# Optimization experiments

Hardware: AMD Instinct MI355X
Metric: run time of the kernel (lower is better)

Reference implementation:

```python
import jax, jax.numpy as jnp
import numpy as np

EMB_DIM = 128
MID = 192  # ceil(1.5 * emb_dim)
VOCAB = 3000
KCLS = 5
B = 16
S = 128
EPS = 1e-5


def _linear_init(k, fin, fout):
    k1, k2 = jax.random.split(k)
    bound = 1.0 / np.sqrt(fin)
    W = jax.random.uniform(k1, (fin, fout), minval=-bound, maxval=bound, dtype=jnp.float32)
    b = jax.random.uniform(k2, (fout,), minval=-bound, maxval=bound, dtype=jnp.float32)
    return W, b


def setup_inputs() -> dict:
    key = jax.random.key(0)
    ks = jax.random.split(key, 7)
    emb = jax.random.normal(ks[0], (VOCAB, EMB_DIM), dtype=jnp.float32)
    W1, b1 = _linear_init(ks[1], 2 * EMB_DIM, MID)   # encoder layer 1
    W2, b2 = _linear_init(ks[2], MID, EMB_DIM)       # encoder layer 2
    W3, b3 = _linear_init(ks[3], EMB_DIM, MID)       # decoder layer 1
    W4, b4 = _linear_init(ks[4], MID, 2 * EMB_DIM)   # decoder layer 2
    Wk, bk = _linear_init(ks[5], EMB_DIM, KCLS)      # soft head
    inputs = jax.random.randint(ks[6], (B, S), 0, VOCAB, dtype=jnp.int64)
    return dict(inputs=inputs, emb=emb, W1=W1, b1=b1, W2=W2, b2=b2,
                W3=W3, b3=b3, W4=W4, b4=b4, Wk=Wk, bk=bk)


def _forward(inputs, emb, W1, b1, W2, b2, W3, b3, W4, b4, Wk, bk):
    X = emb[inputs]                      # (B,S,m)
    Bs, Sl, m = X.shape
    bidx = jnp.arange(Bs)
    karr = jnp.arange(Sl)
    jarr = jnp.arange(Sl - 1)

    def step(carry, t):
        nodes, counts, acc = carry       # (B,S,m), (B,S), (B,)
        L = Sl - t                       # current active list length
        right, left = nodes[:, 1:], nodes[:, :-1]          # pair j = (node[j+1], node[j])
        y = (jnp.concatenate([right, left], -1) @ W1 + b1) @ W2 + b2   # (B,S-1,m)
        xx = (y @ W3 + b3) @ W4 + b4                                    # (B,S-1,2m)
        # torch cross_entropy with float-vector target: -sum(target * log_softmax(input))
        ls1 = -(right * jax.nn.log_softmax(xx[..., :m], -1)).sum(-1)
        ls2 = -(left * jax.nn.log_softmax(xx[..., m:], -1)).sum(-1)
        n1, n2 = counts[:, 1:], counts[:, :-1]
        loss = ((n1 + EPS) * ls1 + (n2 + EPS) * ls2) / (n1 + n2 + EPS)
        valid = jarr < (L - 1)                                          # only first L-1 pairs active
        idx = jnp.argmin(jnp.where(valid[None, :], loss, jnp.inf), axis=1)  # (B,)
        acc = acc + jnp.take_along_axis(loss, idx[:, None], 1)[:, 0]
        father_x = jnp.take_along_axis(y, idx[:, None, None], 1)[:, 0]  # (B,m)
        # faithful bug: lc = nodelist[idx-1] (python wrap to L-1 when idx==0), rc = nodelist[idx]
        lc_idx = jnp.where(idx == 0, L - 1, idx - 1)
        father_cnt = (jnp.take_along_axis(counts, idx[:, None], 1)[:, 0]
                      + jnp.take_along_axis(counts, lc_idx[:, None], 1)[:, 0])
        pos = jnp.maximum(idx - 1, 0)
        # new list: drop lc and rc, father lands at pos; gather map reproduces list insert/remove
        src = jnp.where((idx[:, None] == 0) | (karr[None, :] < idx[:, None] - 1),
                        karr[None, :], karr[None, :] + 1)
        src = jnp.minimum(src, Sl - 1)
        nodes = jnp.take_along_axis(nodes, src[:, :, None], 1).at[bidx, pos].set(father_x)
        counts = jnp.take_along_axis(counts, src, 1).at[bidx, pos].set(father_cnt)
        return (nodes, counts, acc), None

    init = (X, jnp.ones((Bs, Sl), X.dtype), jnp.zeros((Bs,), X.dtype))
    (nodes, counts, acc), _ = jax.lax.scan(step, init, jnp.arange(Sl - 1))
    pred = jnp.argmax(nodes[:, 0] @ Wk + bk, axis=-1)   # argmax softmax == argmax logits
    return pred, acc.sum() / Bs


def reference(inputs, emb, W1, b1, W2, b2, W3, b3, W4, b4, Wk, bk):
    return _forward(inputs, emb, W1, b1, W2, b2, W3, b3, W4, b4, Wk, bk)
```

## Files before the change

kernel.cpp:

```cpp
#include <hip/hip_runtime.h>
#include <math.h>

#define EMB 128
#define MID 192
#define SEQ 128
#define BATCH 16
#define NPAIR 127
#define KCLS 5
#define EPSF 1e-5f

#define OFF_WYT   0
#define OFF_BY    32768
#define OFF_WXXT  32896
#define OFF_BXX   65664
#define OFF_NODES 65920
#define OFF_YC    328064
#define OFF_L0    588160

__global__ void k_comp(const float* __restrict__ W1, const float* __restrict__ b1,
                       const float* __restrict__ W2, const float* __restrict__ b2,
                       const float* __restrict__ W3, const float* __restrict__ b3,
                       const float* __restrict__ W4, const float* __restrict__ b4,
                       float* __restrict__ ws) {
    int tid = blockIdx.x * blockDim.x + threadIdx.x;
    if (tid < 32768) {
        int k = tid >> 7, o = tid & 127;
        float a = 0.f;
        for (int j = 0; j < MID; ++j) a += W1[k*MID+j] * W2[j*EMB+o];
        int q = k >> 6, jj = k & 63;
        ws[OFF_WYT + (size_t)(o*4 + q)*64 + jj] = a;
    } else if (tid < 65536) {
        int t = tid - 32768;
        int k = t >> 8, c = t & 255;
        float a = 0.f;
        for (int j = 0; j < MID; ++j) a += W3[k*MID+j] * W4[j*256+c];
        int hh = k >> 6, jj = k & 63;
        ws[OFF_WXXT + (size_t)(c*2 + hh)*64 + jj] = a;
    } else if (tid < 65536 + 128) {
        int o = tid - 65536;
        float a = b2[o];
        for (int j = 0; j < MID; ++j) a += b1[j] * W2[j*EMB+o];
        ws[OFF_BY + o] = a;
    } else if (tid < 65536 + 128 + 256) {
        int o = tid - 65536 - 128;
        float a = b4[o];
        for (int j = 0; j < MID; ++j) a += b3[j] * W4[j*256+o];
        ws[OFF_BXX + o] = a;
    }
}

__global__ void k_nodes(const int* __restrict__ inp, const float* __restrict__ emb,
                        float* __restrict__ ws) {
    int tid = blockIdx.x * blockDim.x + threadIdx.x;
    if (tid >= BATCH*SEQ*EMB) return;
    int d = tid & 127;
    int bs = tid >> 7;
    int tok = inp[bs];
    ws[OFF_NODES + tid] = emb[tok*EMB + d];
}

#define DPPF(x, ctrl) __int_as_float(__builtin_amdgcn_update_dpp(0, __float_as_int(x), (ctrl), 0xF, 0xF, true))
#define DPPI(x, ctrl) __builtin_amdgcn_update_dpp(0, (x), (ctrl), 0xF, 0xF, true)
#define SWZ16F(x) __int_as_float(__builtin_amdgcn_ds_swizzle(__float_as_int(x), 0x401F))
#define SWZ16I(x) __builtin_amdgcn_ds_swizzle((x), 0x401F)

__global__ void __launch_bounds__(512, 1) k_init(float* __restrict__ ws) {
    __shared__ float s_x[2][2*EMB];
    __shared__ float s_red[4][2][EMB];
    __shared__ float s_redx[2][2][256];
    __shared__ float s_y[2][EMB];
    __shared__ float s_by[EMB];
    __shared__ float s_bxx[2*EMB];
    __shared__ float s_ls[2][2];
    int tid = threadIdx.x;
    int b = blockIdx.x >> 3, g = blockIdx.x & 7;
    float wy[64], wxx[64];
    {
        const float4* gw = (const float4*)(ws + OFF_WYT) + ((size_t)(tid & 127)*4 + (tid >> 7))*16;
        #pragma unroll
        for (int i = 0; i < 16; ++i) { float4 v = gw[i]; wy[4*i]=v.x; wy[4*i+1]=v.y; wy[4*i+2]=v.z; wy[4*i+3]=v.w; }
        const float4* gx = (const float4*)(ws + OFF_WXXT) + ((size_t)(tid & 255)*2 + (tid >> 8))*16;
        #pragma unroll
        for (int i = 0; i < 16; ++i) { float4 v = gx[i]; wxx[4*i]=v.x; wxx[4*i+1]=v.y; wxx[4*i+2]=v.z; wxx[4*i+3]=v.w; }
    }
    if (tid < EMB) s_by[tid] = ws[OFF_BY + tid];
    if (tid < 2*EMB) s_bxx[tid] = ws[OFF_BXX + tid];
    const float* nodes = ws + OFF_NODES + (size_t)b*SEQ*EMB;
    float* yc = ws + OFF_YC + (size_t)b*NPAIR*EMB;
    int q4 = tid >> 7, o = tid & 127;
    int hh = tid >> 8, c = tid & 255;
    int p_s = tid >> 8, kk = tid & 255;
    __syncthreads();
    for (int i = 0; i < 8; ++i) {
        int base = g*16 + i*2;
        {
            int j = base + p_s;
            int jj = j < NPAIR ? j : NPAIR - 1;
            s_x[p_s][kk] = nodes[(jj + (kk < 128 ? 1 : 0))*EMB + (kk & 127)];
        }
        __syncthreads();
        float a0 = 0.f, a1 = 0.f;
        #pragma unroll
        for (int j = 0; j < 64; ++j) {
            float w = wy[j];
            a0 += s_x[0][q4*64 + j] * w;
            a1 += s_x[1][q4*64 + j] * w;
        }
        s_red[q4][0][o] = a0;
        s_red[q4][1][o] = a1;
        __syncthreads();
        if (tid < 256) {
            int p = tid >> 7, oo = tid & 127;
            float yv = s_red[0][p][oo] + s_red[1][p][oo] + s_red[2][p][oo] + s_red[3][p][oo] + s_by[oo];
            s_y[p][oo] = yv;
            int j2 = base + p;
            if (j2 < NPAIR) yc[(size_t)j2*EMB + oo] = yv;
        }
        __syncthreads();
        float c0 = 0.f, c1 = 0.f;
        #pragma unroll
        for (int j = 0; j < 64; ++j) {
            float w = wxx[j];
            c0 += s_y[0][hh*64 + j] * w;
            c1 += s_y[1][hh*64 + j] * w;
        }
        s_redx[hh][0][c] = c0;
        s_redx[hh][1][c] = c1;
        __syncthreads();
        if (tid < 256) {
            int w = tid >> 6, lane = tid & 63;
            int p2 = w >> 1, h2 = w & 1;
            int cA = h2*128 + lane, cB = cA + 64;
            float v0 = s_redx[0][p2][cA] + s_redx[1][p2][cA] + s_bxx[cA];
            float v1 = s_redx[0][p2][cB] + s_redx[1][p2][cB] + s_bxx[cB];
            float m = fmaxf(v0, v1);
            for (int s = 32; s; s >>= 1) m = fmaxf(m, __shfl_xor(m, s, 64));
            float se = expf(v0 - m) + expf(v1 - m);
            for (int s = 32; s; s >>= 1) se += __shfl_xor(se, s, 64);
            float lse = m + logf(se);
            float o0 = s_x[p2][cA], o1 = s_x[p2][cB];
            float term = o0*(v0 - lse) + o1*(v1 - lse);
            for (int s = 32; s; s >>= 1) term += __shfl_xor(term, s, 64);
            if (lane == 0) s_ls[p2][h2] = -term;
        }
        __syncthreads();
        if (tid < 2) {
            int j2 = base + tid;
            if (j2 < NPAIR) {
                float l = ((1.f+EPSF)*s_ls[tid][0] + (1.f+EPSF)*s_ls[tid][1]) / (2.f + EPSF);
                ws[OFF_L0 + b*NPAIR + j2] = l;
            }
        }
        __syncthreads();
    }
}

#define SX(p, c) s_x[p][(((c) >> 6)*72) + ((c) & 63)]

__global__ void __launch_bounds__(512, 1) k_seq(float* __restrict__ ws,
                      const float* __restrict__ Wk, const float* __restrict__ bkv,
                      float* __restrict__ out) {
    __shared__ float s_nodes[SEQ*EMB];
    __shared__ float s_yc[NPAIR*EMB];
    __shared__ float s_x[2][4*72];
    __shared__ float s_y[2][EMB];
    __shared__ float s_xx[2][2*EMB];
    __shared__ float s_by[EMB];
    __shared__ float s_bxx[2*EMB];
    __shared__ float s_ls[2][2];
    __shared__ float s_loss[2][SEQ];
    __shared__ float s_cnt[2][SEQ];
    __shared__ int   s_nslot[2][SEQ];
    __shared__ int   s_yslot[2][SEQ];
    __shared__ float s_restv[4];
    __shared__ int   s_resti[4];
    __shared__ float s_log[KCLS];

    int tid = threadIdx.x;
    int b = blockIdx.x;
    float wy[64], wxx[64];
    {
        const float4* gw = (const float4*)(ws + OFF_WYT) + (size_t)tid*16;
        #pragma unroll
        for (int i = 0; i < 16; ++i) { float4 v = gw[i]; wy[4*i]=v.x; wy[4*i+1]=v.y; wy[4*i+2]=v.z; wy[4*i+3]=v.w; }
        const float4* gx = (const float4*)(ws + OFF_WXXT) + (size_t)tid*16;
        #pragma unroll
        for (int i = 0; i < 16; ++i) { float4 v = gx[i]; wxx[4*i]=v.x; wxx[4*i+1]=v.y; wxx[4*i+2]=v.z; wxx[4*i+3]=v.w; }
    }
    {
        const float4* gn = (const float4*)(ws + OFF_NODES + (size_t)b*SEQ*EMB);
        float4* sn = (float4*)s_nodes;
        for (int i = tid; i < SEQ*EMB/4; i += 512) sn[i] = gn[i];
        const float4* gy = (const float4*)(ws + OFF_YC + (size_t)b*NPAIR*EMB);
        float4* sy = (float4*)s_yc;
        for (int i = tid; i < NPAIR*EMB/4; i += 512) sy[i] = gy[i];
    }
    if (tid < EMB) s_by[tid] = ws[OFF_BY + tid];
    if (tid < 2*EMB) s_bxx[tid] = ws[OFF_BXX + tid];
    if (tid < NPAIR) { s_loss[0][tid] = ws[OFF_L0 + b*NPAIR + tid]; s_yslot[0][tid] = tid; }
    if (tid < SEQ)   { s_cnt[0][tid] = 1.f; s_nslot[0][tid] = tid; }

    float acc = 0.f;
    int cur = 0;
    int q0c = -1, q1c = -1;
    const int q4 = tid & 3,  oy = tid >> 2;
    const int hh = tid & 1,  cx = tid >> 1;
    const int sp = tid >> 8, skk = tid & 255;
    __syncthreads();

    #pragma unroll 1
    for (int t = 0; t < NPAIR; ++t) {
        const int L = SEQ - t;
        if (t > 0) {
            {
                float a0 = 0.f, a1 = 0.f;
                const float* x0 = &s_x[0][q4*72];
                const float* x1 = &s_x[1][q4*72];
                #pragma unroll
                for (int j = 0; j < 64; ++j) { float w = wy[j]; a0 = fmaf(x0[j], w, a0); a1 = fmaf(x1[j], w, a1); }
                a0 += DPPF(a0, 0xB1); a1 += DPPF(a1, 0xB1);
                a0 += DPPF(a0, 0x4E); a1 += DPPF(a1, 0x4E);
                if (q4 == 0) {
                    float bb = s_by[oy];
                    float y0 = a0 + bb, y1 = a1 + bb;
                    s_y[0][oy] = y0; s_y[1][oy] = y1;
                    s_yc[(size_t)s_yslot[cur][q0c]*EMB + oy] = y0;
                    s_yc[(size_t)s_yslot[cur][q1c]*EMB + oy] = y1;
                }
            }
            __syncthreads();
            {
                float c0 = 0.f, c1 = 0.f;
                const float* y0p = &s_y[0][hh*64];
                const float* y1p = &s_y[1][hh*64];
                #pragma unroll
                for (int j = 0; j < 64; ++j) { float w = wxx[j]; c0 = fmaf(y0p[j], w, c0); c1 = fmaf(y1p[j], w, c1); }
                c0 += DPPF(c0, 0xB1); c1 += DPPF(c1, 0xB1);
                if (hh == 0) {
                    float bb = s_bxx[cx];
                    s_xx[0][cx] = c0 + bb;
                    s_xx[1][cx] = c1 + bb;
                }
            }
            __syncthreads();
        }
        if (t > 0 && tid < 128) {
            int p2 = tid >> 6, h2 = (tid >> 5) & 1, l5 = tid & 31;
            int base = h2*128 + l5;
            float v0 = s_xx[p2][base],      v1 = s_xx[p2][base+32];
            float v2 = s_xx[p2][base+64],   v3 = s_xx[p2][base+96];
            float o0 = SX(p2, base),        o1 = SX(p2, base+32);
            float o2 = SX(p2, base+64),     o3 = SX(p2, base+96);
            float m   = fmaxf(fmaxf(v0, v1), fmaxf(v2, v3));
            float sov = v0*o0 + v1*o1 + v2*o2 + v3*o3;
            float so  = (o0 + o1) + (o2 + o3);
            m = fmaxf(m, DPPF(m, 0xB1));  sov += DPPF(sov, 0xB1);  so += DPPF(so, 0xB1);
            m = fmaxf(m, DPPF(m, 0x4E));  sov += DPPF(sov, 0x4E);  so += DPPF(so, 0x4E);
            m = fmaxf(m, DPPF(m, 0x124)); sov += DPPF(sov, 0x124); so += DPPF(so, 0x124);
            m = fmaxf(m, DPPF(m, 0x128)); sov += DPPF(sov, 0x128); so += DPPF(so, 0x128);
            m = fmaxf(m, SWZ16F(m));      sov += SWZ16F(sov);      so += SWZ16F(so);
            float se = expf(v0 - m) + expf(v1 - m) + expf(v2 - m) + expf(v3 - m);
            se += DPPF(se, 0xB1);
            se += DPPF(se, 0x4E);
            se += DPPF(se, 0x124);
            se += DPPF(se, 0x128);
            se += SWZ16F(se);
            if (l5 == 0) s_ls[p2][h2] = (m + logf(se))*so - sov;
        } else if (tid >= 128 && tid < 256) {
            int j = tid - 128;
            float v = (j <= L-2 && j != q0c && j != q1c) ? s_loss[cur][j] : INFINITY;
            int ii = j;
            {   float ov = DPPF(v, 0xB1);  int oi = DPPI(ii, 0xB1);
                bool tk = (ov < v) || (ov == v && oi < ii); v = tk ? ov : v; ii = tk ? oi : ii; }
            {   float ov = DPPF(v, 0x4E);  int oi = DPPI(ii, 0x4E);
                bool tk = (ov < v) || (ov == v && oi < ii); v = tk ? ov : v; ii = tk ? oi : ii; }
            {   float ov = DPPF(v, 0x124); int oi = DPPI(ii, 0x124);
                bool tk = (ov < v) || (ov == v && oi < ii); v = tk ? ov : v; ii = tk ? oi : ii; }
            {   float ov = DPPF(v, 0x128); int oi = DPPI(ii, 0x128);
                bool tk = (ov < v) || (ov == v && oi < ii); v = tk ? ov : v; ii = tk ? oi : ii; }
            {   float ov = SWZ16F(v);      int oi = SWZ16I(ii);
                bool tk = (ov < v) || (ov == v && oi < ii); v = tk ? ov : v; ii = tk ? oi : ii; }
            if ((j & 31) == 0) { s_restv[j >> 5] = v; s_resti[j >> 5] = ii; }
        }
        __syncthreads();
        float l0 = INFINITY, l1 = INFINITY;
        if (t > 0) {
            float n1a = s_cnt[cur][q0c+1], n2a = s_cnt[cur][q0c];
            l0 = ((n1a + EPSF)*s_ls[0][0] + (n2a + EPSF)*s_ls[0][1]) / (n1a + n2a + EPSF);
            float n1b = s_cnt[cur][q1c+1], n2b = s_cnt[cur][q1c];
            l1 = ((n1b + EPSF)*s_ls[1][0] + (n2b + EPSF)*s_ls[1][1]) / (n1b + n2b + EPSF);
        }
        float bv = s_restv[0]; int bi = s_resti[0];
        #pragma unroll
        for (int g = 1; g < 4; ++g) {
            float rv = s_restv[g]; int ri = s_resti[g];
            if (rv < bv || (rv == bv && ri < bi)) { bv = rv; bi = ri; }
        }
        if (t > 0) {
            if (l1 < bv || (l1 == bv && q1c < bi)) { bv = l1; bi = q1c; }
            if (l0 < bv || (l0 == bv && q0c < bi)) { bv = l0; bi = q0c; }
        }
        if (tid == 0) acc += bv;
        const int idx = bi;
        const int pos = idx > 0 ? idx - 1 : 0;
        const bool dS = idx > 0;
        const float fcnt = s_cnt[cur][idx] + s_cnt[cur][idx == 0 ? L-1 : idx-1];
        const int slotFr = s_nslot[cur][pos];
        const int ysIr   = s_yslot[cur][idx];
        const int nxt = cur ^ 1;
        if (tid < NPAIR) {
            int sh = (dS && tid >= pos+1 && tid <= L-3) ? 1 : 0;
            int sj = tid + sh;
            float v = (sj == q0c) ? l0 : (sj == q1c) ? l1 : s_loss[cur][sj];
            s_loss[nxt][tid]  = v;
            s_yslot[nxt][tid] = s_yslot[cur][sj];
        }
        if (tid < SEQ) {
            int sh = (dS && tid >= pos+1 && tid <= L-2) ? 1 : 0;
            s_cnt[nxt][tid]   = (tid == pos) ? fcnt : s_cnt[cur][tid + sh];
            s_nslot[nxt][tid] = s_nslot[cur][tid + sh];
        }
        q0c = pos >= 1 ? pos - 1 : 0;
        q1c = pos;
        if (tid < EMB) s_nodes[slotFr*EMB + tid] = s_yc[(size_t)ysIr*EMB + tid];
        {
            int qq = (sp ? q1c : q0c) + (skk < 128 ? 1 : 0);
            bool sYc = (qq == q1c);
            int sh = (dS && qq >= pos+1 && qq <= L-2) ? 1 : 0;
            int ms = s_nslot[cur][qq + sh];
            float xv = sYc ? s_yc[(size_t)ysIr*EMB + (skk & 127)]
                           : s_nodes[(size_t)ms*EMB + (skk & 127)];
            s_x[sp][((skk >> 6)*72) + (skk & 63)] = xv;
        }
        cur = nxt;
        __syncthreads();
    }
    {
        int w = tid >> 6, l = tid & 63;
        if (w < KCLS) {
            const float* root = s_nodes + (size_t)s_nslot[cur][0]*EMB;
            float p = root[2*l]*Wk[(2*l)*KCLS + w] + root[2*l+1]*Wk[(2*l+1)*KCLS + w];
            for (int s = 32; s; s >>= 1) p += __shfl_xor(p, s, 64);
            if (l == 0) s_log[w] = p + bkv[w];
        }
    }
    __syncthreads();
    if (tid == 0) {
        int best = 0;
        for (int cc = 1; cc < KCLS; ++cc) if (s_log[cc] > s_log[best]) best = cc;
        out[b] = (float)best;
        atomicAdd(&out[BATCH], acc * (1.f/16.f));
    }
}

extern "C" void kernel_launch(void* const* d_in, const int* in_sizes, int n_in,
                              void* d_out, int out_size, void* d_ws, size_t ws_size,
                              hipStream_t stream) {
    const int*   inp = (const int*)d_in[0];
    const float* emb = (const float*)d_in[1];
    const float* W1  = (const float*)d_in[2];
    const float* b1  = (const float*)d_in[3];
    const float* W2  = (const float*)d_in[4];
    const float* b2  = (const float*)d_in[5];
    const float* W3  = (const float*)d_in[6];
    const float* b3  = (const float*)d_in[7];
    const float* W4  = (const float*)d_in[8];
    const float* b4  = (const float*)d_in[9];
    const float* Wk  = (const float*)d_in[10];
    const float* bk  = (const float*)d_in[11];
    float* out = (float*)d_out;
    float* ws  = (float*)d_ws;

    hipMemsetAsync(d_out, 0, (size_t)out_size * sizeof(float), stream);

    k_comp<<<(65920 + 255) / 256, 256, 0, stream>>>(W1, b1, W2, b2, W3, b3, W4, b4, ws);
    k_nodes<<<(BATCH*SEQ*EMB + 255) / 256, 256, 0, stream>>>(inp, emb, ws);
    k_init<<<BATCH * 8, 512, 0, stream>>>(ws);
    k_seq<<<BATCH, 512, 0, stream>>>(ws, Wk, bk, out);
}
```

Before: 504.9 us.

## Double k_seq block to 1024 threads with 32-wide weight chunks per thread

The sequential merge kernel now runs with 1024 threads per block, each holding 32 instead of 64 register weights for the fused encoder and decoder matvecs. Partial sums are reduced across 8 or 4 lanes with DPP and swizzle. The precomputed weight layout changes to 32-element chunks, and k_init is adapted to the new layout. The intent is to shorten the per-step serial dot-product latency on the 127-step critical path, at the cost of larger barriers and an extra cross-lane reduction step.

```diff
diff --git a/kernel.cpp b/kernel.cpp
--- a/kernel.cpp
+++ b/kernel.cpp
@@ -27,15 +27,15 @@
         int k = tid >> 7, o = tid & 127;
         float a = 0.f;
         for (int j = 0; j < MID; ++j) a += W1[k*MID+j] * W2[j*EMB+o];
-        int q = k >> 6, jj = k & 63;
-        ws[OFF_WYT + (size_t)(o*4 + q)*64 + jj] = a;
+        int ch = k >> 5, jj = k & 31;
+        ws[OFF_WYT + (size_t)(o*8 + ch)*32 + jj] = a;
     } else if (tid < 65536) {
         int t = tid - 32768;
         int k = t >> 8, c = t & 255;
         float a = 0.f;
         for (int j = 0; j < MID; ++j) a += W3[k*MID+j] * W4[j*256+c];
-        int hh = k >> 6, jj = k & 63;
-        ws[OFF_WXXT + (size_t)(c*2 + hh)*64 + jj] = a;
+        int ch = k >> 5, jj = k & 31;
+        ws[OFF_WXXT + (size_t)(c*4 + ch)*32 + jj] = a;
     } else if (tid < 65536 + 128) {
         int o = tid - 65536;
         float a = b2[o];
@@ -61,6 +61,7 @@
 
 #define DPPF(x, ctrl) __int_as_float(__builtin_amdgcn_update_dpp(0, __float_as_int(x), (ctrl), 0xF, 0xF, true))
 #define DPPI(x, ctrl) __builtin_amdgcn_update_dpp(0, (x), (ctrl), 0xF, 0xF, true)
+#define SWZ4F(x)  __int_as_float(__builtin_amdgcn_ds_swizzle(__float_as_int(x), 0x101F))
 #define SWZ16F(x) __int_as_float(__builtin_amdgcn_ds_swizzle(__float_as_int(x), 0x401F))
 #define SWZ16I(x) __builtin_amdgcn_ds_swizzle((x), 0x401F)
 
@@ -74,21 +75,27 @@
     __shared__ float s_ls[2][2];
     int tid = threadIdx.x;
     int b = blockIdx.x >> 3, g = blockIdx.x & 7;
+    int q4 = tid >> 7, o = tid & 127;
+    int hh = tid >> 8, c = tid & 255;
     float wy[64], wxx[64];
     {
-        const float4* gw = (const float4*)(ws + OFF_WYT) + ((size_t)(tid & 127)*4 + (tid >> 7))*16;
-        #pragma unroll
-        for (int i = 0; i < 16; ++i) { float4 v = gw[i]; wy[4*i]=v.x; wy[4*i+1]=v.y; wy[4*i+2]=v.z; wy[4*i+3]=v.w; }
-        const float4* gx = (const float4*)(ws + OFF_WXXT) + ((size_t)(tid & 255)*2 + (tid >> 8))*16;
-        #pragma unroll
-        for (int i = 0; i < 16; ++i) { float4 v = gx[i]; wxx[4*i]=v.x; wxx[4*i+1]=v.y; wxx[4*i+2]=v.z; wxx[4*i+3]=v.w; }
+        const float4* gw = (const float4*)(ws + OFF_WYT);
+        #pragma unroll
+        for (int i = 0; i < 16; ++i) {
+            float4 v = gw[((size_t)o*8 + q4*2 + (i>>3))*8 + (i&7)];
+            wy[4*i]=v.x; wy[4*i+1]=v.y; wy[4*i+2]=v.z; wy[4*i+3]=v.w;
+        }
+        const float4* gx = (const float4*)(ws + OFF_WXXT);
+        #pragma unroll
+        for (int i = 0; i < 16; ++i) {
+            float4 v = gx[((size_t)c*4 + hh*2 + (i>>3))*8 + (i&7)];
+            wxx[4*i]=v.x; wxx[4*i+1]=v.y; wxx[4*i+2]=v.z; wxx[4*i+3]=v.w;
+        }
     }
     if (tid < EMB) s_by[tid] = ws[OFF_BY + tid];
     if (tid < 2*EMB) s_bxx[tid] = ws[OFF_BXX + tid];
     const float* nodes = ws + OFF_NODES + (size_t)b*SEQ*EMB;
     float* yc = ws + OFF_YC + (size_t)b*NPAIR*EMB;
-    int q4 = tid >> 7, o = tid & 127;
-    int hh = tid >> 8, c = tid & 255;
     int p_s = tid >> 8, kk = tid & 255;
     __syncthreads();
     for (int i = 0; i < 8; ++i) {
@@ -157,9 +164,10 @@
 
 #define SX(p, c) s_x[p][(((c) >> 6)*72) + ((c) & 63)]
 
-__global__ void __launch_bounds__(512, 1) k_seq(float* __restrict__ ws,
-                      const float* __restrict__ Wk, const float* __restrict__ bkv,
-                      float* __restrict__ out) {
+__global__ void __launch_bounds__(1024, 4) __attribute__((amdgpu_waves_per_eu(4, 4)))
+k_seq(float* __restrict__ ws,
+      const float* __restrict__ Wk, const float* __restrict__ bkv,
+      float* __restrict__ out) {
     __shared__ float s_nodes[SEQ*EMB];
     __shared__ float s_yc[NPAIR*EMB];
     __shared__ float s_x[2][4*72];
@@ -178,22 +186,22 @@
 
     int tid = threadIdx.x;
     int b = blockIdx.x;
-    float wy[64], wxx[64];
+    float wy32[32], wxx32[32];
     {
-        const float4* gw = (const float4*)(ws + OFF_WYT) + (size_t)tid*16;
-        #pragma unroll
-        for (int i = 0; i < 16; ++i) { float4 v = gw[i]; wy[4*i]=v.x; wy[4*i+1]=v.y; wy[4*i+2]=v.z; wy[4*i+3]=v.w; }
-        const float4* gx = (const float4*)(ws + OFF_WXXT) + (size_t)tid*16;
-        #pragma unroll
-        for (int i = 0; i < 16; ++i) { float4 v = gx[i]; wxx[4*i]=v.x; wxx[4*i+1]=v.y; wxx[4*i+2]=v.z; wxx[4*i+3]=v.w; }
+        const float4* gw = (const float4*)(ws + OFF_WYT) + (size_t)tid*8;
+        #pragma unroll
+        for (int i = 0; i < 8; ++i) { float4 v = gw[i]; wy32[4*i]=v.x; wy32[4*i+1]=v.y; wy32[4*i+2]=v.z; wy32[4*i+3]=v.w; }
+        const float4* gx = (const float4*)(ws + OFF_WXXT) + (size_t)tid*8;
+        #pragma unroll
+        for (int i = 0; i < 8; ++i) { float4 v = gx[i]; wxx32[4*i]=v.x; wxx32[4*i+1]=v.y; wxx32[4*i+2]=v.z; wxx32[4*i+3]=v.w; }
     }
     {
         const float4* gn = (const float4*)(ws + OFF_NODES + (size_t)b*SEQ*EMB);
         float4* sn = (float4*)s_nodes;
-        for (int i = tid; i < SEQ*EMB/4; i += 512) sn[i] = gn[i];
+        for (int i = tid; i < SEQ*EMB/4; i += 1024) sn[i] = gn[i];
         const float4* gy = (const float4*)(ws + OFF_YC + (size_t)b*NPAIR*EMB);
         float4* sy = (float4*)s_yc;
-        for (int i = tid; i < NPAIR*EMB/4; i += 512) sy[i] = gy[i];
+        for (int i = tid; i < NPAIR*EMB/4; i += 1024) sy[i] = gy[i];
     }
     if (tid < EMB) s_by[tid] = ws[OFF_BY + tid];
     if (tid < 2*EMB) s_bxx[tid] = ws[OFF_BXX + tid];
@@ -203,8 +211,8 @@
     float acc = 0.f;
     int cur = 0;
     int q0c = -1, q1c = -1;
-    const int q4 = tid & 3,  oy = tid >> 2;
-    const int hh = tid & 1,  cx = tid >> 1;
+    const int ch1 = tid & 7,  o1 = tid >> 3;
+    const int ch2 = tid & 3,  c2 = tid >> 2;
     const int sp = tid >> 8, skk = tid & 255;
     __syncthreads();
 
@@ -214,32 +222,34 @@
         if (t > 0) {
             {
                 float a0 = 0.f, a1 = 0.f;
-                const float* x0 = &s_x[0][q4*72];
-                const float* x1 = &s_x[1][q4*72];
+                const float* x0 = &s_x[0][(ch1 >> 1)*72 + (ch1 & 1)*32];
+                const float* x1 = &s_x[1][(ch1 >> 1)*72 + (ch1 & 1)*32];
                 #pragma unroll
-                for (int j = 0; j < 64; ++j) { float w = wy[j]; a0 = fmaf(x0[j], w, a0); a1 = fmaf(x1[j], w, a1); }
+                for (int j = 0; j < 32; ++j) { float w = wy32[j]; a0 = fmaf(x0[j], w, a0); a1 = fmaf(x1[j], w, a1); }
                 a0 += DPPF(a0, 0xB1); a1 += DPPF(a1, 0xB1);
                 a0 += DPPF(a0, 0x4E); a1 += DPPF(a1, 0x4E);
-                if (q4 == 0) {
-                    float bb = s_by[oy];
+                a0 += SWZ4F(a0);      a1 += SWZ4F(a1);
+                if (ch1 == 0) {
+                    float bb = s_by[o1];
                     float y0 = a0 + bb, y1 = a1 + bb;
-                    s_y[0][oy] = y0; s_y[1][oy] = y1;
-                    s_yc[(size_t)s_yslot[cur][q0c]*EMB + oy] = y0;
-                    s_yc[(size_t)s_yslot[cur][q1c]*EMB + oy] = y1;
+                    s_y[0][o1] = y0; s_y[1][o1] = y1;
+                    s_yc[(size_t)s_yslot[cur][q0c]*EMB + o1] = y0;
+                    s_yc[(size_t)s_yslot[cur][q1c]*EMB + o1] = y1;
                 }
             }
             __syncthreads();
             {
                 float c0 = 0.f, c1 = 0.f;
-                const float* y0p = &s_y[0][hh*64];
-                const float* y1p = &s_y[1][hh*64];
+                const float* y0p = &s_y[0][ch2*32];
+                const float* y1p = &s_y[1][ch2*32];
                 #pragma unroll
-                for (int j = 0; j < 64; ++j) { float w = wxx[j]; c0 = fmaf(y0p[j], w, c0); c1 = fmaf(y1p[j], w, c1); }
+                for (int j = 0; j < 32; ++j) { float w = wxx32[j]; c0 = fmaf(y0p[j], w, c0); c1 = fmaf(y1p[j], w, c1); }
                 c0 += DPPF(c0, 0xB1); c1 += DPPF(c1, 0xB1);
-                if (hh == 0) {
-                    float bb = s_bxx[cx];
-                    s_xx[0][cx] = c0 + bb;
-                    s_xx[1][cx] = c1 + bb;
+                c0 += DPPF(c0, 0x4E); c1 += DPPF(c1, 0x4E);
+                if (ch2 == 0) {
+                    float bb = s_bxx[c2];
+                    s_xx[0][c2] = c0 + bb;
+                    s_xx[1][c2] = c1 + bb;
                 }
             }
             __syncthreads();
@@ -249,11 +259,11 @@
             int base = h2*128 + l5;
             float v0 = s_xx[p2][base],      v1 = s_xx[p2][base+32];
             float v2 = s_xx[p2][base+64],   v3 = s_xx[p2][base+96];
-            float o0 = SX(p2, base),        o1 = SX(p2, base+32);
+            float o0 = SX(p2, base),        o1v = SX(p2, base+32);
             float o2 = SX(p2, base+64),     o3 = SX(p2, base+96);
             float m   = fmaxf(fmaxf(v0, v1), fmaxf(v2, v3));
-            float sov = v0*o0 + v1*o1 + v2*o2 + v3*o3;
-            float so  = (o0 + o1) + (o2 + o3);
+            float sov = v0*o0 + v1*o1v + v2*o2 + v3*o3;
+            float so  = (o0 + o1v) + (o2 + o3);
             m = fmaxf(m, DPPF(m, 0xB1));  sov += DPPF(sov, 0xB1);  so += DPPF(so, 0xB1);
             m = fmaxf(m, DPPF(m, 0x4E));  sov += DPPF(sov, 0x4E);  so += DPPF(so, 0x4E);
             m = fmaxf(m, DPPF(m, 0x124)); sov += DPPF(sov, 0x124); so += DPPF(so, 0x124);
@@ -323,7 +333,7 @@
         q0c = pos >= 1 ? pos - 1 : 0;
         q1c = pos;
         if (tid < EMB) s_nodes[slotFr*EMB + tid] = s_yc[(size_t)ysIr*EMB + tid];
-        {
+        if (tid < 512) {
             int qq = (sp ? q1c : q0c) + (skk < 128 ? 1 : 0);
             bool sYc = (qq == q1c);
             int sh = (dS && qq >= pos+1 && qq <= L-2) ? 1 : 0;
@@ -376,5 +386,5 @@
     k_comp<<<(65920 + 255) / 256, 256, 0, stream>>>(W1, b1, W2, b2, W3, b3, W4, b4, ws);
     k_nodes<<<(BATCH*SEQ*EMB + 255) / 256, 256, 0, stream>>>(inp, emb, ws);
     k_init<<<BATCH * 8, 512, 0, stream>>>(ws);
-    k_seq<<<BATCH, 512, 0, stream>>>(ws, Wk, bk, out);
-}
+    k_seq<<<BATCH, 1024, 0, stream>>>(ws, Wk, bk, out);
+}
```

Measured after the change: 524.2 us. +3.8%, slower.

## Move decoder weights into LDS and node/pair storage to global memory in k_seq

Applied to the files above, without the earlier changes.

The sequential merge kernel now keeps the fused decoder weight matrix in shared memory (row-padded to 132 floats) and reads it with float4 loads, instead of holding 64 weights per thread in registers. The node and pair-embedding arrays, which used to live in shared memory, are now read and written directly in the global workspace. This is meant to cut register pressure. In exchange, every serial step now does global loads and stores, and the write-then-read of global memory within a block relies on __syncthreads for visibility, which adds latency to the dependent chain.

```diff
diff --git a/kernel.cpp b/kernel.cpp
--- a/kernel.cpp
+++ b/kernel.cpp
@@ -34,8 +34,7 @@
         int k = t >> 8, c = t & 255;
         float a = 0.f;
         for (int j = 0; j < MID; ++j) a += W3[k*MID+j] * W4[j*256+c];
-        int hh = k >> 6, jj = k & 63;
-        ws[OFF_WXXT + (size_t)(c*2 + hh)*64 + jj] = a;
+        ws[OFF_WXXT + (size_t)c*128 + k] = a;
     } else if (tid < 65536 + 128) {
         int o = tid - 65536;
         float a = b2[o];
@@ -74,12 +73,14 @@
     __shared__ float s_ls[2][2];
     int tid = threadIdx.x;
     int b = blockIdx.x >> 3, g = blockIdx.x & 7;
+    int q4 = tid >> 7, o = tid & 127;
+    int hh = tid >> 8, c = tid & 255;
     float wy[64], wxx[64];
     {
-        const float4* gw = (const float4*)(ws + OFF_WYT) + ((size_t)(tid & 127)*4 + (tid >> 7))*16;
+        const float4* gw = (const float4*)(ws + OFF_WYT) + ((size_t)(o*4 + q4))*16;
         #pragma unroll
         for (int i = 0; i < 16; ++i) { float4 v = gw[i]; wy[4*i]=v.x; wy[4*i+1]=v.y; wy[4*i+2]=v.z; wy[4*i+3]=v.w; }
-        const float4* gx = (const float4*)(ws + OFF_WXXT) + ((size_t)(tid & 255)*2 + (tid >> 8))*16;
+        const float4* gx = (const float4*)(ws + OFF_WXXT) + ((size_t)c*32 + hh*16);
         #pragma unroll
         for (int i = 0; i < 16; ++i) { float4 v = gx[i]; wxx[4*i]=v.x; wxx[4*i+1]=v.y; wxx[4*i+2]=v.z; wxx[4*i+3]=v.w; }
     }
@@ -87,8 +88,6 @@
     if (tid < 2*EMB) s_bxx[tid] = ws[OFF_BXX + tid];
     const float* nodes = ws + OFF_NODES + (size_t)b*SEQ*EMB;
     float* yc = ws + OFF_YC + (size_t)b*NPAIR*EMB;
-    int q4 = tid >> 7, o = tid & 127;
-    int hh = tid >> 8, c = tid & 255;
     int p_s = tid >> 8, kk = tid & 255;
     __syncthreads();
     for (int i = 0; i < 8; ++i) {
@@ -160,8 +159,7 @@
 __global__ void __launch_bounds__(512, 1) k_seq(float* __restrict__ ws,
                       const float* __restrict__ Wk, const float* __restrict__ bkv,
                       float* __restrict__ out) {
-    __shared__ float s_nodes[SEQ*EMB];
-    __shared__ float s_yc[NPAIR*EMB];
+    __shared__ float s_wxx[256*132];
     __shared__ float s_x[2][4*72];
     __shared__ float s_y[2][EMB];
     __shared__ float s_xx[2][2*EMB];
@@ -178,22 +176,21 @@
 
     int tid = threadIdx.x;
     int b = blockIdx.x;
-    float wy[64], wxx[64];
+    float* gn  = ws + OFF_NODES + (size_t)b*SEQ*EMB;
+    float* gyc = ws + OFF_YC   + (size_t)b*NPAIR*EMB;
+
+    float wy[64];
     {
         const float4* gw = (const float4*)(ws + OFF_WYT) + (size_t)tid*16;
         #pragma unroll
         for (int i = 0; i < 16; ++i) { float4 v = gw[i]; wy[4*i]=v.x; wy[4*i+1]=v.y; wy[4*i+2]=v.z; wy[4*i+3]=v.w; }
-        const float4* gx = (const float4*)(ws + OFF_WXXT) + (size_t)tid*16;
-        #pragma unroll
-        for (int i = 0; i < 16; ++i) { float4 v = gx[i]; wxx[4*i]=v.x; wxx[4*i+1]=v.y; wxx[4*i+2]=v.z; wxx[4*i+3]=v.w; }
     }
     {
-        const float4* gn = (const float4*)(ws + OFF_NODES + (size_t)b*SEQ*EMB);
-        float4* sn = (float4*)s_nodes;
-        for (int i = tid; i < SEQ*EMB/4; i += 512) sn[i] = gn[i];
-        const float4* gy = (const float4*)(ws + OFF_YC + (size_t)b*NPAIR*EMB);
-        float4* sy = (float4*)s_yc;
-        for (int i = tid; i < NPAIR*EMB/4; i += 512) sy[i] = gy[i];
+        const float* gx = ws + OFF_WXXT;
+        for (int i = tid; i < 256*128; i += 512) {
+            int c = i >> 7, k = i & 127;
+            s_wxx[c*132 + k] = gx[i];
+        }
     }
     if (tid < EMB) s_by[tid] = ws[OFF_BY + tid];
     if (tid < 2*EMB) s_bxx[tid] = ws[OFF_BXX + tid];
@@ -224,17 +221,26 @@
                     float bb = s_by[oy];
                     float y0 = a0 + bb, y1 = a1 + bb;
                     s_y[0][oy] = y0; s_y[1][oy] = y1;
-                    s_yc[(size_t)s_yslot[cur][q0c]*EMB + oy] = y0;
-                    s_yc[(size_t)s_yslot[cur][q1c]*EMB + oy] = y1;
+                    gyc[(size_t)s_yslot[cur][q0c]*EMB + oy] = y0;
+                    gyc[(size_t)s_yslot[cur][q1c]*EMB + oy] = y1;
                 }
             }
             __syncthreads();
             {
                 float c0 = 0.f, c1 = 0.f;
-                const float* y0p = &s_y[0][hh*64];
-                const float* y1p = &s_y[1][hh*64];
+                const float4* wr  = (const float4*)(s_wxx + (size_t)cx*132 + hh*64);
+                const float4* y0q = (const float4*)(&s_y[0][hh*64]);
+                const float4* y1q = (const float4*)(&s_y[1][hh*64]);
                 #pragma unroll
-                for (int j = 0; j < 64; ++j) { float w = wxx[j]; c0 = fmaf(y0p[j], w, c0); c1 = fmaf(y1p[j], w, c1); }
+                for (int i = 0; i < 16; ++i) {
+                    float4 w4 = wr[i];
+                    float4 u0 = y0q[i];
+                    float4 u1 = y1q[i];
+                    c0 = fmaf(u0.x, w4.x, c0); c1 = fmaf(u1.x, w4.x, c1);
+                    c0 = fmaf(u0.y, w4.y, c0); c1 = fmaf(u1.y, w4.y, c1);
+                    c0 = fmaf(u0.z, w4.z, c0); c1 = fmaf(u1.z, w4.z, c1);
+                    c0 = fmaf(u0.w, w4.w, c0); c1 = fmaf(u1.w, w4.w, c1);
+                }
                 c0 += DPPF(c0, 0xB1); c1 += DPPF(c1, 0xB1);
                 if (hh == 0) {
                     float bb = s_bxx[cx];
@@ -249,11 +255,11 @@
             int base = h2*128 + l5;
             float v0 = s_xx[p2][base],      v1 = s_xx[p2][base+32];
             float v2 = s_xx[p2][base+64],   v3 = s_xx[p2][base+96];
-            float o0 = SX(p2, base),        o1 = SX(p2, base+32);
+            float o0 = SX(p2, base),        o1v = SX(p2, base+32);
             float o2 = SX(p2, base+64),     o3 = SX(p2, base+96);
             float m   = fmaxf(fmaxf(v0, v1), fmaxf(v2, v3));
-            float sov = v0*o0 + v1*o1 + v2*o2 + v3*o3;
-            float so  = (o0 + o1) + (o2 + o3);
+            float sov = v0*o0 + v1*o1v + v2*o2 + v3*o3;
+            float so  = (o0 + o1v) + (o2 + o3);
             m = fmaxf(m, DPPF(m, 0xB1));  sov += DPPF(sov, 0xB1);  so += DPPF(so, 0xB1);
             m = fmaxf(m, DPPF(m, 0x4E));  sov += DPPF(sov, 0x4E);  so += DPPF(so, 0x4E);
             m = fmaxf(m, DPPF(m, 0x124)); sov += DPPF(sov, 0x124); so += DPPF(so, 0x124);
@@ -322,14 +328,14 @@
         }
         q0c = pos >= 1 ? pos - 1 : 0;
         q1c = pos;
-        if (tid < EMB) s_nodes[slotFr*EMB + tid] = s_yc[(size_t)ysIr*EMB + tid];
+        if (tid < EMB) gn[(size_t)slotFr*EMB + tid] = gyc[(size_t)ysIr*EMB + tid];
         {
             int qq = (sp ? q1c : q0c) + (skk < 128 ? 1 : 0);
             bool sYc = (qq == q1c);
             int sh = (dS && qq >= pos+1 && qq <= L-2) ? 1 : 0;
             int ms = s_nslot[cur][qq + sh];
-            float xv = sYc ? s_yc[(size_t)ysIr*EMB + (skk & 127)]
-                           : s_nodes[(size_t)ms*EMB + (skk & 127)];
+            float xv = sYc ? gyc[(size_t)ysIr*EMB + (skk & 127)]
+                           : gn[(size_t)ms*EMB + (skk & 127)];
             s_x[sp][((skk >> 6)*72) + (skk & 63)] = xv;
         }
         cur = nxt;
@@ -338,7 +344,7 @@
     {
         int w = tid >> 6, l = tid & 63;
         if (w < KCLS) {
-            const float* root = s_nodes + (size_t)s_nslot[cur][0]*EMB;
+            const float* root = gn + (size_t)s_nslot[cur][0]*EMB;
             float p = root[2*l]*Wk[(2*l)*KCLS + w] + root[2*l+1]*Wk[(2*l+1)*KCLS + w];
             for (int s = 32; s; s >>= 1) p += __shfl_xor(p, s, 64);
             if (l == 0) s_log[w] = p + bkv[w];
```

Result: slower. 574.8 us (+13.8%).
